# Kernel optimization log

Measured on AMD Instinct MI355X. Metric: run time of the kernel, lower is better.

The kernel has to match this reference:

```python
import jax, jax.numpy as jnp
import numpy as np

NF, NH1, NH21, NH22, NCLS = 6, 128, 128, 128, 3
OBS_X, OBS_Y, OBS_Z, R = 10.0, 10.0, 9.0, 7.0
BATCH = 131072


def setup_inputs() -> dict:
    key = jax.random.key(0)
    ks = jax.random.split(key, 16)
    def lin(kw, kb, fan_in, fan_out):
        bound = 1.0 / np.sqrt(fan_in)
        w = jax.random.uniform(kw, (fan_out, fan_in), jnp.float32, -bound, bound)
        b = jax.random.uniform(kb, (fan_out,), jnp.float32, -bound, bound)
        return w, b
    fc1_w, fc1_b = lin(ks[0], ks[1], NF, NH1)
    fc21_w, fc21_b = lin(ks[2], ks[3], NH1, NH21)
    fc22_w, fc22_b = lin(ks[4], ks[5], NH1, NH22)
    fcm1_w, fcm1_b = lin(ks[6], ks[7], NH21, NH21)
    fcm2_w, fcm2_b = lin(ks[8], ks[9], NH22, NH22)
    fc31_w, fc31_b = lin(ks[10], ks[11], NH21, NCLS)
    fc32_w, fc32_b = lin(ks[12], ks[13], NH22, 2)
    x = jax.random.normal(ks[14], (BATCH, NF), jnp.float32)
    mean = jnp.array([10.0, 0.0, 10.0, 0.0, 9.0, 0.0], jnp.float32)
    std = jnp.array([5.0, 2.0, 5.0, 2.0, 5.0, 2.0], jnp.float32)
    return {"x": x, "mean": mean, "std": std,
            "fc1_w": fc1_w, "fc1_b": fc1_b,
            "fc21_w": fc21_w, "fc21_b": fc21_b,
            "fc22_w": fc22_w, "fc22_b": fc22_b,
            "fcm1_w": fcm1_w, "fcm1_b": fcm1_b,
            "fcm2_w": fcm2_w, "fcm2_b": fcm2_b,
            "fc31_w": fc31_w, "fc31_b": fc31_b,
            "fc32_w": fc32_w, "fc32_b": fc32_b,
            "sgn": 1}


def _forward(x, mean, std, fc1_w, fc1_b, fc21_w, fc21_b, fc22_w, fc22_b,
             fcm1_w, fcm1_b, fcm2_w, fcm2_b, fc31_w, fc31_b, fc32_w, fc32_b):
    x0 = x * std + mean                                   # de-normalized state [B,6]
    h = jnp.tanh(x @ fc1_w.T + fc1_b)                     # [B,NH1]
    x21 = jnp.tanh(h @ fc21_w.T + fc21_b)
    x22 = jnp.tanh(h @ fc22_w.T + fc22_b)
    x21 = jnp.tanh(x21 @ fcm1_w.T + fcm1_b)
    x22 = jnp.tanh(x22 @ fcm2_w.T + fcm2_b)
    x31 = x21 @ fc31_w.T + fc31_b                         # QP linear term p, [B,3]
    x32 = 4.0 * jax.nn.sigmoid(x22 @ fc32_w.T + fc32_b)   # HOCBF penalties, [B,2]

    # higher-order CBF terms
    px, vx, py, vy, pz, vz = (x0[:, i] for i in range(6))
    dx, dy, dz = px - OBS_X, py - OBS_Y, pz - OBS_Z
    barrier = dx**4 + dy**4 + dz**4 - R**4
    barrier_dot = 4.0 * (dx**3 * vx + dy**3 * vy + dz**3 * vz)
    Lf2b = 12.0 * (dx**2 * vx**2 + dy**2 * vy**2 + dz**2 * vz**2)
    G = -4.0 * jnp.stack([dx**3, dy**3, dz**3], axis=-1)  # [B,3], single constraint G u <= h
    hvec = Lf2b + (x32[:, 0] + x32[:, 1]) * barrier_dot + x32[:, 0] * x32[:, 1] * barrier  # [B]

    # QP: min 0.5 u^T u + x31^T u  s.t.  G u <= h  (Q = I, one constraint)
    # Closed-form KKT: u = -x31 - lam*G, lam = max(0, (G @ (-x31) - h) / (G @ G))
    u_unc = -x31
    Gu = jnp.sum(G * u_unc, axis=-1)                      # [B]
    GG = jnp.sum(G * G, axis=-1)                          # [B]
    lam = jnp.maximum(Gu - hvec, 0.0) / GG
    u = u_unc - lam[:, None] * G                          # [B,3]
    return u


def reference(x, mean, std, fc1_w, fc1_b, fc21_w, fc21_b, fc22_w, fc22_b,
              fcm1_w, fcm1_b, fcm2_w, fcm2_b, fc31_w, fc31_b, fc32_w, fc32_b, sgn):
    return _forward(x, mean, std, fc1_w, fc1_b, fc21_w, fc21_b, fc22_w, fc22_b,
                    fcm1_w, fcm1_b, fcm2_w, fcm2_b, fc31_w, fc31_b, fc32_w, fc32_b)
```

## Files before the change

kernel.cpp:

```cpp
#include <hip/hip_runtime.h>

typedef _Float16 half8 __attribute__((ext_vector_type(8)));
typedef _Float16 half4_t __attribute__((ext_vector_type(4)));
typedef __fp16 fp16x2 __attribute__((ext_vector_type(2)));
typedef float float4_t __attribute__((ext_vector_type(4)));
typedef float float2_t __attribute__((ext_vector_type(2)));

#define SB 64
#define NT 512
#define RS (SB * 8)

#define OFF_W1   0
#define OFF_W21  4096
#define OFF_W22  20480
#define OFF_WM1  36864
#define OFF_WM2  53248
#define OFF_W4A  69632
#define OFF_BIAS 73728
#define WS_HELEMS 73728

#define SCL_TANH 2.8853900817779268f
#define SCL_SIG  -1.4426950408889634f

__device__ __forceinline__ float tanh_pre(float a) {
  float e = __builtin_amdgcn_exp2f(a);
  return fmaf(-2.f, __builtin_amdgcn_rcpf(1.f + e), 1.f);
}
__device__ __forceinline__ half4_t pack4(float v0, float v1, float v2, float v3) {
  fp16x2 lo = __builtin_amdgcn_cvt_pkrtz(v0, v1);
  fp16x2 hi = __builtin_amdgcn_cvt_pkrtz(v2, v3);
  half4_t h;
  h[0] = (_Float16)lo[0]; h[1] = (_Float16)lo[1];
  h[2] = (_Float16)hi[0]; h[3] = (_Float16)hi[1];
  return h;
}

__global__ void prepack(const float* __restrict__ w1, const float* __restrict__ w21,
                        const float* __restrict__ w22, const float* __restrict__ wm1,
                        const float* __restrict__ wm2, const float* __restrict__ w31,
                        const float* __restrict__ w32, const float* __restrict__ b1,
                        const float* __restrict__ b21, const float* __restrict__ b22,
                        const float* __restrict__ bm1, const float* __restrict__ bm2,
                        _Float16* __restrict__ ws) {
  const int stride = gridDim.x * blockDim.x;
  for (int i = blockIdx.x * blockDim.x + threadIdx.x; i < WS_HELEMS; i += stride) {
    float v;
    if (i < OFF_W21) {
      int t = i;
      int j = t & 7, c = t >> 3, l16 = c & 15, t1 = c >> 4;
      int k8 = t1 & 3, mt = t1 >> 2;
      int row = mt * 16 + l16, k = k8 * 8 + j;
      v = (k < 6) ? w1[row * 6 + k] * SCL_TANH : 0.f;
    } else if (i < OFF_W4A) {
      int t = i - OFF_W21;
      int m = t >> 14; t &= 16383;
      const float* src = (m == 0) ? w21 : (m == 1) ? w22 : (m == 2) ? wm1 : wm2;
      int j = t & 7, c = t >> 3, l16 = c & 15, t1 = c >> 4;
      int k8 = t1 & 15, mt = t1 >> 4;
      v = src[(mt * 16 + l16) * 128 + k8 * 8 + j] * SCL_TANH;
    } else {
      int t = i - OFF_W4A;
      int j = t & 7, r = t >> 3, l16 = r & 15, q = r >> 4;
      int cc = q & 15, chain = q >> 4;
      int k = cc * 8 + j, m = l16;
      if (chain == 0) v = (m < 3) ? w31[m * 128 + k] : 0.f;
      else            v = (m < 2) ? w32[m * 128 + k] * SCL_SIG : 0.f;
    }
    ws[i] = (_Float16)v;
  }
  float* bws = (float*)(ws + OFF_BIAS);
  for (int i = blockIdx.x * blockDim.x + threadIdx.x; i < 640; i += stride) {
    int layer = i >> 7, idx = i & 127;
    const float* src = (layer == 0) ? b1 : (layer == 1) ? b21
                     : (layer == 2) ? b22 : (layer == 3) ? bm1 : bm2;
    bws[i] = src[idx] * SCL_TANH;
  }
}

__device__ __forceinline__ void layer128(const half8* __restrict__ A, float4_t bv,
                                         const _Float16* __restrict__ inB,
                                         _Float16* __restrict__ outB,
                                         int quad, int l16, int wv) {
  float4_t acc[4];
  acc[0] = bv; acc[1] = bv; acc[2] = bv; acc[3] = bv;
#pragma unroll
  for (int kk = 0; kk < 4; ++kk) {
#pragma unroll
    for (int nt = 0; nt < 4; ++nt) {
      half8 b = *(const half8*)(inB + (kk * 4 + quad) * RS + (nt * 16 + l16) * 8);
      acc[nt] = __builtin_amdgcn_mfma_f32_16x16x32_f16(A[kk], b, acc[nt], 0, 0, 0);
    }
  }
  const int ob = wv * 16 + quad * 4;
  _Float16* base = outB + (ob >> 3) * RS + (ob & 7);
#pragma unroll
  for (int nt = 0; nt < 4; ++nt) {
    const int s = nt * 16 + l16;
    half4_t h = pack4(tanh_pre(acc[nt][0]), tanh_pre(acc[nt][1]),
                      tanh_pre(acc[nt][2]), tanh_pre(acc[nt][3]));
    *(half4_t*)(base + s * 8) = h;
  }
}

__global__ __launch_bounds__(NT, 3) void bnet_main(
    const float* __restrict__ x, const float* __restrict__ meang,
    const float* __restrict__ stdg, const float* __restrict__ b31,
    const float* __restrict__ b32, const _Float16* __restrict__ ws,
    float* __restrict__ out) {
  __shared__ __align__(16) _Float16 bufH[SB * 128];
  __shared__ __align__(16) _Float16 bufA[SB * 128];
  __shared__ __align__(16) _Float16 bufB[SB * 128];

  const int tid = threadIdx.x;
  const int wv = tid >> 6;
  const int lane = tid & 63;
  const int quad = lane >> 4;
  const int l16 = lane & 15;
  const int s0 = blockIdx.x * SB;
  const float* biasF = (const float*)(ws + OFF_BIAS);
  const int arow = (wv * 16 + quad * 4);

  half8 A1 = *(const half8*)(ws + OFF_W1 + ((wv * 4 + quad) * 16 + l16) * 8);
  float4_t bv1 = *(const float4_t*)(biasF + arow);
  float4_t bv21 = *(const float4_t*)(biasF + 128 + arow);
  float4_t bv22 = *(const float4_t*)(biasF + 256 + arow);
  float4_t bvm1 = *(const float4_t*)(biasF + 384 + arow);
  float4_t bvm2 = *(const float4_t*)(biasF + 512 + arow);
  half8 A21[4];
#pragma unroll
  for (int kk = 0; kk < 4; ++kk)
    A21[kk] = *(const half8*)(ws + OFF_W21 + ((wv * 16 + kk * 4 + quad) * 16 + l16) * 8);

  {
    float4_t acc[4];
    acc[0] = bv1; acc[1] = bv1; acc[2] = bv1; acc[3] = bv1;
#pragma unroll
    for (int nt = 0; nt < 4; ++nt) {
      half8 v;
#pragma unroll
      for (int j = 0; j < 8; ++j) v[j] = (_Float16)0.f;
      if (quad == 0) {
        const float* xp = x + (size_t)(s0 + nt * 16 + l16) * 6;
        float2_t e0 = *(const float2_t*)(xp);
        float2_t e1 = *(const float2_t*)(xp + 2);
        float2_t e2 = *(const float2_t*)(xp + 4);
        v[0] = (_Float16)e0[0]; v[1] = (_Float16)e0[1];
        v[2] = (_Float16)e1[0]; v[3] = (_Float16)e1[1];
        v[4] = (_Float16)e2[0]; v[5] = (_Float16)e2[1];
      }
      acc[nt] = __builtin_amdgcn_mfma_f32_16x16x32_f16(A1, v, acc[nt], 0, 0, 0);
    }
    _Float16* base = bufH + (arow >> 3) * RS + (arow & 7);
#pragma unroll
    for (int nt = 0; nt < 4; ++nt) {
      const int s = nt * 16 + l16;
      half4_t h = pack4(tanh_pre(acc[nt][0]), tanh_pre(acc[nt][1]),
                        tanh_pre(acc[nt][2]), tanh_pre(acc[nt][3]));
      *(half4_t*)(base + s * 8) = h;
    }
  }
  half8 A22[4];
#pragma unroll
  for (int kk = 0; kk < 4; ++kk)
    A22[kk] = *(const half8*)(ws + OFF_W22 + ((wv * 16 + kk * 4 + quad) * 16 + l16) * 8);
  __syncthreads();

  layer128(A21, bv21, bufH, bufA, quad, l16, wv);
  half8 AM1[4];
#pragma unroll
  for (int kk = 0; kk < 4; ++kk)
    AM1[kk] = *(const half8*)(ws + OFF_WM1 + ((wv * 16 + kk * 4 + quad) * 16 + l16) * 8);
  layer128(A22, bv22, bufH, bufB, quad, l16, wv);
  half8 AM2[4];
#pragma unroll
  for (int kk = 0; kk < 4; ++kk)
    AM2[kk] = *(const half8*)(ws + OFF_WM2 + ((wv * 16 + kk * 4 + quad) * 16 + l16) * 8);
  __syncthreads();

  layer128(AM1, bvm1, bufA, bufH, quad, l16, wv);
  half8 A4[2][4];
  if (wv < 4) {
#pragma unroll
    for (int c = 0; c < 2; ++c)
#pragma unroll
      for (int kk = 0; kk < 4; ++kk)
        A4[c][kk] = *(const half8*)(ws + OFF_W4A +
                                    ((c * 16 + kk * 4 + quad) * 16 + l16) * 8);
  }
  __syncthreads();

  layer128(AM2, bvm2, bufB, bufA, quad, l16, wv);
  __syncthreads();

  if (wv < 4) {
    const int nt = wv;
    float4_t c0 = (float4_t){0.f, 0.f, 0.f, 0.f};
    float4_t c1 = (float4_t){0.f, 0.f, 0.f, 0.f};
    if (quad == 0) {
      c0[0] = b31[0]; c0[1] = b31[1]; c0[2] = b31[2];
      c1[0] = b32[0] * SCL_SIG; c1[1] = b32[1] * SCL_SIG;
    }
#pragma unroll
    for (int kk = 0; kk < 4; ++kk) {
      half8 bh = *(const half8*)(bufH + (kk * 4 + quad) * RS + (nt * 16 + l16) * 8);
      half8 bc = *(const half8*)(bufA + (kk * 4 + quad) * RS + (nt * 16 + l16) * 8);
      c0 = __builtin_amdgcn_mfma_f32_16x16x32_f16(A4[0][kk], bh, c0, 0, 0, 0);
      c1 = __builtin_amdgcn_mfma_f32_16x16x32_f16(A4[1][kk], bc, c1, 0, 0, 0);
    }
    if (quad == 0) {
      const int s = nt * 16 + l16;
      float u0 = -c0[0];
      float u1 = -c0[1];
      float u2 = -c0[2];
      float p0 = 4.f * __builtin_amdgcn_rcpf(1.f + __builtin_amdgcn_exp2f(c1[0]));
      float p1 = 4.f * __builtin_amdgcn_rcpf(1.f + __builtin_amdgcn_exp2f(c1[1]));
      const float m0 = meang[0], m1 = meang[1], m2 = meang[2];
      const float m3 = meang[3], m4 = meang[4], m5 = meang[5];
      const float sd0 = stdg[0], sd1 = stdg[1], sd2 = stdg[2];
      const float sd3 = stdg[3], sd4 = stdg[4], sd5 = stdg[5];
      const float* xp = x + (size_t)(s0 + s) * 6;
      float2_t e0 = *(const float2_t*)(xp);
      float2_t e1 = *(const float2_t*)(xp + 2);
      float2_t e2 = *(const float2_t*)(xp + 4);
      float px = e0[0] * sd0 + m0, vx = e0[1] * sd1 + m1;
      float py = e1[0] * sd2 + m2, vy = e1[1] * sd3 + m3;
      float pz = e2[0] * sd4 + m4, vz = e2[1] * sd5 + m5;
      float dx = px - 10.f, dy = py - 10.f, dz = pz - 9.f;
      float dx2 = dx * dx, dy2 = dy * dy, dz2 = dz * dz;
      float dx3 = dx2 * dx, dy3 = dy2 * dy, dz3 = dz2 * dz;
      float barrier = dx3 * dx + dy3 * dy + dz3 * dz - 2401.f;
      float bdot = 4.f * (dx3 * vx + dy3 * vy + dz3 * vz);
      float Lf2b = 12.f * (dx2 * vx * vx + dy2 * vy * vy + dz2 * vz * vz);
      float g0 = -4.f * dx3, g1 = -4.f * dy3, g2 = -4.f * dz3;
      float hv = Lf2b + (p0 + p1) * bdot + p0 * p1 * barrier;
      float Gu = g0 * u0 + g1 * u1 + g2 * u2;
      float GG = g0 * g0 + g1 * g1 + g2 * g2;
      float lam = fmaxf(Gu - hv, 0.f) / GG;
      float* op = out + (size_t)(s0 + s) * 3;
      op[0] = u0 - lam * g0;
      op[1] = u1 - lam * g1;
      op[2] = u2 - lam * g2;
    }
  }
}

extern "C" void kernel_launch(void* const* d_in, const int* in_sizes, int n_in,
                              void* d_out, int out_size, void* d_ws, size_t ws_size,
                              hipStream_t stream) {
  const float* x    = (const float*)d_in[0];
  const float* mean = (const float*)d_in[1];
  const float* stdv = (const float*)d_in[2];
  const float* w1   = (const float*)d_in[3];
  const float* b1   = (const float*)d_in[4];
  const float* w21  = (const float*)d_in[5];
  const float* b21  = (const float*)d_in[6];
  const float* w22  = (const float*)d_in[7];
  const float* b22  = (const float*)d_in[8];
  const float* wm1  = (const float*)d_in[9];
  const float* bm1  = (const float*)d_in[10];
  const float* wm2  = (const float*)d_in[11];
  const float* bm2  = (const float*)d_in[12];
  const float* w31  = (const float*)d_in[13];
  const float* b31  = (const float*)d_in[14];
  const float* w32  = (const float*)d_in[15];
  const float* b32  = (const float*)d_in[16];
  _Float16* ws = (_Float16*)d_ws;
  float* out = (float*)d_out;
  const int batch = in_sizes[0] / 6;

  hipLaunchKernelGGL(prepack, dim3(96), dim3(256), 0, stream,
                     w1, w21, w22, wm1, wm2, w31, w32,
                     b1, b21, b22, bm1, bm2, ws);
  hipLaunchKernelGGL(bnet_main, dim3(batch / SB), dim3(NT), 0, stream,
                     x, mean, stdv, b31, b32, (const _Float16*)ws, out);
}
```

Before: 123.5 us.

## Restructure MLP so each wave owns 32 samples with LDS-staged weights

Changes the work split so that each wave computes all 128 output features for its own 32 samples, instead of every wave computing a 16-row output slice for the block's shared 64 samples. Layer weights are staged into double-buffered LDS, and the next layer's weights are loaded while the current layer runs. Activations stay in a private per-wave padded slab and are read back as MFMA fragments, which removes most of the inter-wave dependence on block-wide activation buffers. Each block now covers 256 samples, launch bounds drop to one block per CU, and the LDS footprint grows, so latency hiding rests on fewer resident waves.

```diff
diff --git a/kernel.cpp b/kernel.cpp
--- a/kernel.cpp
+++ b/kernel.cpp
@@ -6,9 +6,10 @@
 typedef float float4_t __attribute__((ext_vector_type(4)));
 typedef float float2_t __attribute__((ext_vector_type(2)));
 
-#define SB 64
 #define NT 512
-#define RS (SB * 8)
+#define SW 32
+#define SBLK 256
+#define P 136
 
 #define OFF_W1   0
 #define OFF_W21  4096
@@ -77,169 +78,191 @@
   }
 }
 
-__device__ __forceinline__ void layer128(const half8* __restrict__ A, float4_t bv,
-                                         const _Float16* __restrict__ inB,
-                                         _Float16* __restrict__ outB,
-                                         int quad, int l16, int wv) {
-  float4_t acc[4];
-  acc[0] = bv; acc[1] = bv; acc[2] = bv; acc[3] = bv;
-#pragma unroll
-  for (int kk = 0; kk < 4; ++kk) {
-#pragma unroll
-    for (int nt = 0; nt < 4; ++nt) {
-      half8 b = *(const half8*)(inB + (kk * 4 + quad) * RS + (nt * 16 + l16) * 8);
-      acc[nt] = __builtin_amdgcn_mfma_f32_16x16x32_f16(A[kk], b, acc[nt], 0, 0, 0);
-    }
-  }
-  const int ob = wv * 16 + quad * 4;
-  _Float16* base = outB + (ob >> 3) * RS + (ob & 7);
-#pragma unroll
-  for (int nt = 0; nt < 4; ++nt) {
-    const int s = nt * 16 + l16;
-    half4_t h = pack4(tanh_pre(acc[nt][0]), tanh_pre(acc[nt][1]),
-                      tanh_pre(acc[nt][2]), tanh_pre(acc[nt][3]));
-    *(half4_t*)(base + s * 8) = h;
-  }
-}
-
-__global__ __launch_bounds__(NT, 3) void bnet_main(
+__device__ __forceinline__ void stage32(const _Float16* __restrict__ src,
+                                        _Float16* __restrict__ dst, int tid) {
+#pragma unroll
+  for (int i = 0; i < 4; ++i)
+    *(half8*)(dst + (i * NT + tid) * 8) = *(const half8*)(src + (i * NT + tid) * 8);
+}
+__device__ __forceinline__ void stage8(const _Float16* __restrict__ src,
+                                       _Float16* __restrict__ dst, int tid) {
+  *(half8*)(dst + tid * 8) = *(const half8*)(src + tid * 8);
+}
+
+__device__ __forceinline__ void layer_big(const _Float16* __restrict__ wb,
+                                          const float* __restrict__ bbase,
+                                          const half8 (&bIn)[2][4],
+                                          _Float16* __restrict__ myslab,
+                                          int quad, int l16) {
+#pragma unroll
+  for (int m = 0; m < 8; ++m) {
+    float4_t bv = *(const float4_t*)(bbase + m * 16 + quad * 4);
+    float4_t a0 = bv, a1 = bv;
+#pragma unroll
+    for (int kk = 0; kk < 4; ++kk) {
+      half8 A = *(const half8*)(wb + ((m * 16 + kk * 4 + quad) * 16 + l16) * 8);
+      a0 = __builtin_amdgcn_mfma_f32_16x16x32_f16(A, bIn[0][kk], a0, 0, 0, 0);
+      a1 = __builtin_amdgcn_mfma_f32_16x16x32_f16(A, bIn[1][kk], a1, 0, 0, 0);
+    }
+    const int fo = m * 16 + quad * 4;
+    *(half4_t*)(myslab + l16 * P + fo) =
+        pack4(tanh_pre(a0[0]), tanh_pre(a0[1]), tanh_pre(a0[2]), tanh_pre(a0[3]));
+    *(half4_t*)(myslab + (16 + l16) * P + fo) =
+        pack4(tanh_pre(a1[0]), tanh_pre(a1[1]), tanh_pre(a1[2]), tanh_pre(a1[3]));
+  }
+}
+
+__device__ __forceinline__ void read_frags(const _Float16* __restrict__ myslab,
+                                           half8 (&bOut)[2][4], int quad, int l16) {
+  asm volatile("s_waitcnt lgkmcnt(0)" ::: "memory");
+  __builtin_amdgcn_sched_barrier(0);
+#pragma unroll
+  for (int n = 0; n < 2; ++n)
+#pragma unroll
+    for (int kk = 0; kk < 4; ++kk)
+      bOut[n][kk] = *(const half8*)(myslab + (n * 16 + l16) * P + kk * 32 + quad * 8);
+}
+
+__global__ __launch_bounds__(NT, 1) void bnet_main(
     const float* __restrict__ x, const float* __restrict__ meang,
     const float* __restrict__ stdg, const float* __restrict__ b31,
     const float* __restrict__ b32, const _Float16* __restrict__ ws,
     float* __restrict__ out) {
-  __shared__ __align__(16) _Float16 bufH[SB * 128];
-  __shared__ __align__(16) _Float16 bufA[SB * 128];
-  __shared__ __align__(16) _Float16 bufB[SB * 128];
+  __shared__ __align__(16) _Float16 wb0[16384];
+  __shared__ __align__(16) _Float16 wb1[16384];
+  __shared__ __align__(16) _Float16 slab[8 * SW * P];
+  __shared__ __align__(16) float bbuf[640];
 
   const int tid = threadIdx.x;
   const int wv = tid >> 6;
   const int lane = tid & 63;
   const int quad = lane >> 4;
   const int l16 = lane & 15;
-  const int s0 = blockIdx.x * SB;
+  const int s0w = blockIdx.x * SBLK + wv * SW;
   const float* biasF = (const float*)(ws + OFF_BIAS);
-  const int arow = (wv * 16 + quad * 4);
-
-  half8 A1 = *(const half8*)(ws + OFF_W1 + ((wv * 4 + quad) * 16 + l16) * 8);
-  float4_t bv1 = *(const float4_t*)(biasF + arow);
-  float4_t bv21 = *(const float4_t*)(biasF + 128 + arow);
-  float4_t bv22 = *(const float4_t*)(biasF + 256 + arow);
-  float4_t bvm1 = *(const float4_t*)(biasF + 384 + arow);
-  float4_t bvm2 = *(const float4_t*)(biasF + 512 + arow);
-  half8 A21[4];
-#pragma unroll
-  for (int kk = 0; kk < 4; ++kk)
-    A21[kk] = *(const half8*)(ws + OFF_W21 + ((wv * 16 + kk * 4 + quad) * 16 + l16) * 8);
+  _Float16* myslab = slab + wv * (SW * P);
+
+  stage8(ws + OFF_W1, wb0, tid);
+  stage32(ws + OFF_W21, wb1, tid);
+  bbuf[tid] = biasF[tid];
+  if (tid < 128) bbuf[512 + tid] = biasF[512 + tid];
+  __syncthreads();
+
+  half8 xb[2];
+#pragma unroll
+  for (int n = 0; n < 2; ++n) {
+#pragma unroll
+    for (int j = 0; j < 8; ++j) xb[n][j] = (_Float16)0.f;
+    if (quad == 0) {
+      const float* xp = x + (size_t)(s0w + n * 16 + l16) * 6;
+      float2_t e0 = *(const float2_t*)(xp);
+      float2_t e1 = *(const float2_t*)(xp + 2);
+      float2_t e2 = *(const float2_t*)(xp + 4);
+      xb[n][0] = (_Float16)e0[0]; xb[n][1] = (_Float16)e0[1];
+      xb[n][2] = (_Float16)e1[0]; xb[n][3] = (_Float16)e1[1];
+      xb[n][4] = (_Float16)e2[0]; xb[n][5] = (_Float16)e2[1];
+    }
+  }
+#pragma unroll
+  for (int m = 0; m < 8; ++m) {
+    float4_t bv = *(const float4_t*)(bbuf + m * 16 + quad * 4);
+    float4_t a0 = bv, a1 = bv;
+    half8 A = *(const half8*)(wb0 + ((m * 4 + quad) * 16 + l16) * 8);
+    a0 = __builtin_amdgcn_mfma_f32_16x16x32_f16(A, xb[0], a0, 0, 0, 0);
+    a1 = __builtin_amdgcn_mfma_f32_16x16x32_f16(A, xb[1], a1, 0, 0, 0);
+    const int fo = m * 16 + quad * 4;
+    *(half4_t*)(myslab + l16 * P + fo) =
+        pack4(tanh_pre(a0[0]), tanh_pre(a0[1]), tanh_pre(a0[2]), tanh_pre(a0[3]));
+    *(half4_t*)(myslab + (16 + l16) * P + fo) =
+        pack4(tanh_pre(a1[0]), tanh_pre(a1[1]), tanh_pre(a1[2]), tanh_pre(a1[3]));
+  }
+  half8 f_h[2][4];
+  read_frags(myslab, f_h, quad, l16);
+  __syncthreads();
+
+  stage32(ws + OFF_W22, wb0, tid);
+  layer_big(wb1, bbuf + 128, f_h, myslab, quad, l16);
+  half8 f_a[2][4];
+  read_frags(myslab, f_a, quad, l16);
+  __syncthreads();
+
+  stage32(ws + OFF_WM1, wb1, tid);
+  layer_big(wb0, bbuf + 256, f_h, myslab, quad, l16);
+  half8 f_b[2][4];
+  read_frags(myslab, f_b, quad, l16);
+  __syncthreads();
+
+  stage32(ws + OFF_WM2, wb0, tid);
+  layer_big(wb1, bbuf + 384, f_a, myslab, quad, l16);
+  read_frags(myslab, f_a, quad, l16);
+  __syncthreads();
+
+  stage8(ws + OFF_W4A, wb1, tid);
+  layer_big(wb0, bbuf + 512, f_b, myslab, quad, l16);
+  read_frags(myslab, f_b, quad, l16);
+  __syncthreads();
 
   {
-    float4_t acc[4];
-    acc[0] = bv1; acc[1] = bv1; acc[2] = bv1; acc[3] = bv1;
-#pragma unroll
-    for (int nt = 0; nt < 4; ++nt) {
-      half8 v;
-#pragma unroll
-      for (int j = 0; j < 8; ++j) v[j] = (_Float16)0.f;
+    half8 A40[4], A41[4];
+#pragma unroll
+    for (int kk = 0; kk < 4; ++kk) {
+      A40[kk] = *(const half8*)(wb1 + ((kk * 4 + quad) * 16 + l16) * 8);
+      A41[kk] = *(const half8*)(wb1 + ((16 + kk * 4 + quad) * 16 + l16) * 8);
+    }
+    float4_t c0[2], c1[2];
+#pragma unroll
+    for (int n = 0; n < 2; ++n) {
+      c0[n] = (float4_t){0.f, 0.f, 0.f, 0.f};
+      c1[n] = (float4_t){0.f, 0.f, 0.f, 0.f};
       if (quad == 0) {
-        const float* xp = x + (size_t)(s0 + nt * 16 + l16) * 6;
-        float2_t e0 = *(const float2_t*)(xp);
-        float2_t e1 = *(const float2_t*)(xp + 2);
-        float2_t e2 = *(const float2_t*)(xp + 4);
-        v[0] = (_Float16)e0[0]; v[1] = (_Float16)e0[1];
-        v[2] = (_Float16)e1[0]; v[3] = (_Float16)e1[1];
-        v[4] = (_Float16)e2[0]; v[5] = (_Float16)e2[1];
+        c0[n][0] = b31[0]; c0[n][1] = b31[1]; c0[n][2] = b31[2];
+        c1[n][0] = b32[0] * SCL_SIG; c1[n][1] = b32[1] * SCL_SIG;
       }
-      acc[nt] = __builtin_amdgcn_mfma_f32_16x16x32_f16(A1, v, acc[nt], 0, 0, 0);
-    }
-    _Float16* base = bufH + (arow >> 3) * RS + (arow & 7);
-#pragma unroll
-    for (int nt = 0; nt < 4; ++nt) {
-      const int s = nt * 16 + l16;
-      half4_t h = pack4(tanh_pre(acc[nt][0]), tanh_pre(acc[nt][1]),
-                        tanh_pre(acc[nt][2]), tanh_pre(acc[nt][3]));
-      *(half4_t*)(base + s * 8) = h;
-    }
-  }
-  half8 A22[4];
-#pragma unroll
-  for (int kk = 0; kk < 4; ++kk)
-    A22[kk] = *(const half8*)(ws + OFF_W22 + ((wv * 16 + kk * 4 + quad) * 16 + l16) * 8);
-  __syncthreads();
-
-  layer128(A21, bv21, bufH, bufA, quad, l16, wv);
-  half8 AM1[4];
-#pragma unroll
-  for (int kk = 0; kk < 4; ++kk)
-    AM1[kk] = *(const half8*)(ws + OFF_WM1 + ((wv * 16 + kk * 4 + quad) * 16 + l16) * 8);
-  layer128(A22, bv22, bufH, bufB, quad, l16, wv);
-  half8 AM2[4];
-#pragma unroll
-  for (int kk = 0; kk < 4; ++kk)
-    AM2[kk] = *(const half8*)(ws + OFF_WM2 + ((wv * 16 + kk * 4 + quad) * 16 + l16) * 8);
-  __syncthreads();
-
-  layer128(AM1, bvm1, bufA, bufH, quad, l16, wv);
-  half8 A4[2][4];
-  if (wv < 4) {
-#pragma unroll
-    for (int c = 0; c < 2; ++c)
-#pragma unroll
-      for (int kk = 0; kk < 4; ++kk)
-        A4[c][kk] = *(const half8*)(ws + OFF_W4A +
-                                    ((c * 16 + kk * 4 + quad) * 16 + l16) * 8);
-  }
-  __syncthreads();
-
-  layer128(AM2, bvm2, bufB, bufA, quad, l16, wv);
-  __syncthreads();
-
-  if (wv < 4) {
-    const int nt = wv;
-    float4_t c0 = (float4_t){0.f, 0.f, 0.f, 0.f};
-    float4_t c1 = (float4_t){0.f, 0.f, 0.f, 0.f};
+    }
+#pragma unroll
+    for (int kk = 0; kk < 4; ++kk) {
+#pragma unroll
+      for (int n = 0; n < 2; ++n) {
+        c0[n] = __builtin_amdgcn_mfma_f32_16x16x32_f16(A40[kk], f_a[n][kk], c0[n], 0, 0, 0);
+        c1[n] = __builtin_amdgcn_mfma_f32_16x16x32_f16(A41[kk], f_b[n][kk], c1[n], 0, 0, 0);
+      }
+    }
     if (quad == 0) {
-      c0[0] = b31[0]; c0[1] = b31[1]; c0[2] = b31[2];
-      c1[0] = b32[0] * SCL_SIG; c1[1] = b32[1] * SCL_SIG;
-    }
-#pragma unroll
-    for (int kk = 0; kk < 4; ++kk) {
-      half8 bh = *(const half8*)(bufH + (kk * 4 + quad) * RS + (nt * 16 + l16) * 8);
-      half8 bc = *(const half8*)(bufA + (kk * 4 + quad) * RS + (nt * 16 + l16) * 8);
-      c0 = __builtin_amdgcn_mfma_f32_16x16x32_f16(A4[0][kk], bh, c0, 0, 0, 0);
-      c1 = __builtin_amdgcn_mfma_f32_16x16x32_f16(A4[1][kk], bc, c1, 0, 0, 0);
-    }
-    if (quad == 0) {
-      const int s = nt * 16 + l16;
-      float u0 = -c0[0];
-      float u1 = -c0[1];
-      float u2 = -c0[2];
-      float p0 = 4.f * __builtin_amdgcn_rcpf(1.f + __builtin_amdgcn_exp2f(c1[0]));
-      float p1 = 4.f * __builtin_amdgcn_rcpf(1.f + __builtin_amdgcn_exp2f(c1[1]));
       const float m0 = meang[0], m1 = meang[1], m2 = meang[2];
       const float m3 = meang[3], m4 = meang[4], m5 = meang[5];
       const float sd0 = stdg[0], sd1 = stdg[1], sd2 = stdg[2];
       const float sd3 = stdg[3], sd4 = stdg[4], sd5 = stdg[5];
-      const float* xp = x + (size_t)(s0 + s) * 6;
-      float2_t e0 = *(const float2_t*)(xp);
-      float2_t e1 = *(const float2_t*)(xp + 2);
-      float2_t e2 = *(const float2_t*)(xp + 4);
-      float px = e0[0] * sd0 + m0, vx = e0[1] * sd1 + m1;
-      float py = e1[0] * sd2 + m2, vy = e1[1] * sd3 + m3;
-      float pz = e2[0] * sd4 + m4, vz = e2[1] * sd5 + m5;
-      float dx = px - 10.f, dy = py - 10.f, dz = pz - 9.f;
-      float dx2 = dx * dx, dy2 = dy * dy, dz2 = dz * dz;
-      float dx3 = dx2 * dx, dy3 = dy2 * dy, dz3 = dz2 * dz;
-      float barrier = dx3 * dx + dy3 * dy + dz3 * dz - 2401.f;
-      float bdot = 4.f * (dx3 * vx + dy3 * vy + dz3 * vz);
-      float Lf2b = 12.f * (dx2 * vx * vx + dy2 * vy * vy + dz2 * vz * vz);
-      float g0 = -4.f * dx3, g1 = -4.f * dy3, g2 = -4.f * dz3;
-      float hv = Lf2b + (p0 + p1) * bdot + p0 * p1 * barrier;
-      float Gu = g0 * u0 + g1 * u1 + g2 * u2;
-      float GG = g0 * g0 + g1 * g1 + g2 * g2;
-      float lam = fmaxf(Gu - hv, 0.f) / GG;
-      float* op = out + (size_t)(s0 + s) * 3;
-      op[0] = u0 - lam * g0;
-      op[1] = u1 - lam * g1;
-      op[2] = u2 - lam * g2;
+#pragma unroll
+      for (int n = 0; n < 2; ++n) {
+        const int s = s0w + n * 16 + l16;
+        float u0 = -c0[n][0];
+        float u1 = -c0[n][1];
+        float u2 = -c0[n][2];
+        float p0 = 4.f * __builtin_amdgcn_rcpf(1.f + __builtin_amdgcn_exp2f(c1[n][0]));
+        float p1 = 4.f * __builtin_amdgcn_rcpf(1.f + __builtin_amdgcn_exp2f(c1[n][1]));
+        const float* xp = x + (size_t)s * 6;
+        float2_t e0 = *(const float2_t*)(xp);
+        float2_t e1 = *(const float2_t*)(xp + 2);
+        float2_t e2 = *(const float2_t*)(xp + 4);
+        float px = e0[0] * sd0 + m0, vx = e0[1] * sd1 + m1;
+        float py = e1[0] * sd2 + m2, vy = e1[1] * sd3 + m3;
+        float pz = e2[0] * sd4 + m4, vz = e2[1] * sd5 + m5;
+        float dx = px - 10.f, dy = py - 10.f, dz = pz - 9.f;
+        float dx2 = dx * dx, dy2 = dy * dy, dz2 = dz * dz;
+        float dx3 = dx2 * dx, dy3 = dy2 * dy, dz3 = dz2 * dz;
+        float barrier = dx3 * dx + dy3 * dy + dz3 * dz - 2401.f;
+        float bdot = 4.f * (dx3 * vx + dy3 * vy + dz3 * vz);
+        float Lf2b = 12.f * (dx2 * vx * vx + dy2 * vy * vy + dz2 * vz * vz);
+        float g0 = -4.f * dx3, g1 = -4.f * dy3, g2 = -4.f * dz3;
+        float hv = Lf2b + (p0 + p1) * bdot + p0 * p1 * barrier;
+        float Gu = g0 * u0 + g1 * u1 + g2 * u2;
+        float GG = g0 * g0 + g1 * g1 + g2 * g2;
+        float lam = fmaxf(Gu - hv, 0.f) / GG;
+        float* op = out + (size_t)s * 3;
+        op[0] = u0 - lam * g0;
+        op[1] = u1 - lam * g1;
+        op[2] = u2 - lam * g2;
+      }
     }
   }
 }
@@ -271,6 +294,6 @@
   hipLaunchKernelGGL(prepack, dim3(96), dim3(256), 0, stream,
                      w1, w21, w22, wm1, wm2, w31, w32,
                      b1, b21, b22, bm1, bm2, ws);
-  hipLaunchKernelGGL(bnet_main, dim3(batch / SB), dim3(NT), 0, stream,
+  hipLaunchKernelGGL(bnet_main, dim3(batch / SBLK), dim3(NT), 0, stream,
                      x, mean, stdv, b31, b32, (const _Float16*)ws, out);
 }
```

After: 124.1 us. No clear change (+0.5%).

## Retile hidden layers as 2x2 MFMA warp tiles with just-in-time weight loads

Applied to the files above, without the earlier changes.

Each 128-wide hidden layer was split as one 16-row output tile per wave across all four 16-sample column tiles. It is now a 2x2 block per wave: two output-row tiles times two sample tiles. Each B fragment read from LDS now feeds two MFMAs, which halves LDS reads per MFMA. Weights and biases are loaded inside the layer instead of being prefetched one layer ahead, and the bias is added after accumulation. Occupancy hint drops from 3 to 2 blocks per CU, which gives more registers but exposes weight-load latency that prefetching used to hide.

```diff
diff --git a/kernel.cpp b/kernel.cpp
--- a/kernel.cpp
+++ b/kernel.cpp
@@ -77,32 +77,59 @@
   }
 }
 
-__device__ __forceinline__ void layer128(const half8* __restrict__ A, float4_t bv,
+__device__ __forceinline__ void layer2x2(const _Float16* __restrict__ wA,
+                                         const float* __restrict__ bb,
                                          const _Float16* __restrict__ inB,
                                          _Float16* __restrict__ outB,
-                                         int quad, int l16, int wv) {
-  float4_t acc[4];
-  acc[0] = bv; acc[1] = bv; acc[2] = bv; acc[3] = bv;
-#pragma unroll
-  for (int kk = 0; kk < 4; ++kk) {
-#pragma unroll
-    for (int nt = 0; nt < 4; ++nt) {
-      half8 b = *(const half8*)(inB + (kk * 4 + quad) * RS + (nt * 16 + l16) * 8);
-      acc[nt] = __builtin_amdgcn_mfma_f32_16x16x32_f16(A[kk], b, acc[nt], 0, 0, 0);
-    }
-  }
-  const int ob = wv * 16 + quad * 4;
-  _Float16* base = outB + (ob >> 3) * RS + (ob & 7);
-#pragma unroll
-  for (int nt = 0; nt < 4; ++nt) {
-    const int s = nt * 16 + l16;
-    half4_t h = pack4(tanh_pre(acc[nt][0]), tanh_pre(acc[nt][1]),
-                      tanh_pre(acc[nt][2]), tanh_pre(acc[nt][3]));
-    *(half4_t*)(base + s * 8) = h;
-  }
-}
-
-__global__ __launch_bounds__(NT, 3) void bnet_main(
+                                         int mg, int ng, int quad, int l16) {
+  const int mt0 = mg * 2;
+  half8 A[2][4];
+#pragma unroll
+  for (int mi = 0; mi < 2; ++mi)
+#pragma unroll
+    for (int kk = 0; kk < 4; ++kk)
+      A[mi][kk] = *(const half8*)(wA + (((mt0 + mi) * 16 + kk * 4 + quad) * 16 + l16) * 8);
+  float4_t bv[2];
+  bv[0] = *(const float4_t*)(bb + (mt0 + 0) * 16 + quad * 4);
+  bv[1] = *(const float4_t*)(bb + (mt0 + 1) * 16 + quad * 4);
+
+  float4_t acc[2][2];
+#pragma unroll
+  for (int mi = 0; mi < 2; ++mi)
+#pragma unroll
+    for (int ni = 0; ni < 2; ++ni)
+      acc[mi][ni] = (float4_t){0.f, 0.f, 0.f, 0.f};
+
+#pragma unroll
+  for (int ni = 0; ni < 2; ++ni) {
+    const int nt = ng * 2 + ni;
+    half8 B[4];
+#pragma unroll
+    for (int kk = 0; kk < 4; ++kk)
+      B[kk] = *(const half8*)(inB + (kk * 4 + quad) * RS + (nt * 16 + l16) * 8);
+#pragma unroll
+    for (int kk = 0; kk < 4; ++kk) {
+      acc[0][ni] = __builtin_amdgcn_mfma_f32_16x16x32_f16(A[0][kk], B[kk], acc[0][ni], 0, 0, 0);
+      acc[1][ni] = __builtin_amdgcn_mfma_f32_16x16x32_f16(A[1][kk], B[kk], acc[1][ni], 0, 0, 0);
+    }
+  }
+
+#pragma unroll
+  for (int mi = 0; mi < 2; ++mi) {
+    const int ob = (mt0 + mi) * 16 + quad * 4;
+    _Float16* base = outB + (ob >> 3) * RS + (ob & 7);
+#pragma unroll
+    for (int ni = 0; ni < 2; ++ni) {
+      const int s = (ng * 2 + ni) * 16 + l16;
+      float4_t a = acc[mi][ni];
+      half4_t h = pack4(tanh_pre(a[0] + bv[mi][0]), tanh_pre(a[1] + bv[mi][1]),
+                        tanh_pre(a[2] + bv[mi][2]), tanh_pre(a[3] + bv[mi][3]));
+      *(half4_t*)(base + s * 8) = h;
+    }
+  }
+}
+
+__global__ __launch_bounds__(NT, 2) void bnet_main(
     const float* __restrict__ x, const float* __restrict__ meang,
     const float* __restrict__ stdg, const float* __restrict__ b31,
     const float* __restrict__ b32, const _Float16* __restrict__ ws,
@@ -116,68 +143,64 @@
   const int lane = tid & 63;
   const int quad = lane >> 4;
   const int l16 = lane & 15;
+  const int mg = wv >> 1;
+  const int ng = wv & 1;
   const int s0 = blockIdx.x * SB;
   const float* biasF = (const float*)(ws + OFF_BIAS);
-  const int arow = (wv * 16 + quad * 4);
-
-  half8 A1 = *(const half8*)(ws + OFF_W1 + ((wv * 4 + quad) * 16 + l16) * 8);
-  float4_t bv1 = *(const float4_t*)(biasF + arow);
-  float4_t bv21 = *(const float4_t*)(biasF + 128 + arow);
-  float4_t bv22 = *(const float4_t*)(biasF + 256 + arow);
-  float4_t bvm1 = *(const float4_t*)(biasF + 384 + arow);
-  float4_t bvm2 = *(const float4_t*)(biasF + 512 + arow);
-  half8 A21[4];
-#pragma unroll
-  for (int kk = 0; kk < 4; ++kk)
-    A21[kk] = *(const half8*)(ws + OFF_W21 + ((wv * 16 + kk * 4 + quad) * 16 + l16) * 8);
 
   {
-    float4_t acc[4];
-    acc[0] = bv1; acc[1] = bv1; acc[2] = bv1; acc[3] = bv1;
-#pragma unroll
-    for (int nt = 0; nt < 4; ++nt) {
-      half8 v;
-#pragma unroll
-      for (int j = 0; j < 8; ++j) v[j] = (_Float16)0.f;
+    half8 A1[2];
+#pragma unroll
+    for (int mi = 0; mi < 2; ++mi)
+      A1[mi] = *(const half8*)(ws + OFF_W1 + (((mg * 2 + mi) * 4 + quad) * 16 + l16) * 8);
+    float4_t bv1[2];
+    bv1[0] = *(const float4_t*)(biasF + (mg * 2 + 0) * 16 + quad * 4);
+    bv1[1] = *(const float4_t*)(biasF + (mg * 2 + 1) * 16 + quad * 4);
+
+    half8 xb[2];
+#pragma unroll
+    for (int ni = 0; ni < 2; ++ni) {
+#pragma unroll
+      for (int j = 0; j < 8; ++j) xb[ni][j] = (_Float16)0.f;
       if (quad == 0) {
-        const float* xp = x + (size_t)(s0 + nt * 16 + l16) * 6;
+        const float* xp = x + (size_t)(s0 + (ng * 2 + ni) * 16 + l16) * 6;
         float2_t e0 = *(const float2_t*)(xp);
         float2_t e1 = *(const float2_t*)(xp + 2);
         float2_t e2 = *(const float2_t*)(xp + 4);
-        v[0] = (_Float16)e0[0]; v[1] = (_Float16)e0[1];
-        v[2] = (_Float16)e1[0]; v[3] = (_Float16)e1[1];
-        v[4] = (_Float16)e2[0]; v[5] = (_Float16)e2[1];
+        xb[ni][0] = (_Float16)e0[0]; xb[ni][1] = (_Float16)e0[1];
+        xb[ni][2] = (_Float16)e1[0]; xb[ni][3] = (_Float16)e1[1];
+        xb[ni][4] = (_Float16)e2[0]; xb[ni][5] = (_Float16)e2[1];
       }
-      acc[nt] = __builtin_amdgcn_mfma_f32_16x16x32_f16(A1, v, acc[nt], 0, 0, 0);
-    }
-    _Float16* base = bufH + (arow >> 3) * RS + (arow & 7);
-#pragma unroll
-    for (int nt = 0; nt < 4; ++nt) {
-      const int s = nt * 16 + l16;
-      half4_t h = pack4(tanh_pre(acc[nt][0]), tanh_pre(acc[nt][1]),
-                        tanh_pre(acc[nt][2]), tanh_pre(acc[nt][3]));
-      *(half4_t*)(base + s * 8) = h;
-    }
-  }
-  half8 A22[4];
-#pragma unroll
-  for (int kk = 0; kk < 4; ++kk)
-    A22[kk] = *(const half8*)(ws + OFF_W22 + ((wv * 16 + kk * 4 + quad) * 16 + l16) * 8);
-  __syncthreads();
-
-  layer128(A21, bv21, bufH, bufA, quad, l16, wv);
-  half8 AM1[4];
-#pragma unroll
-  for (int kk = 0; kk < 4; ++kk)
-    AM1[kk] = *(const half8*)(ws + OFF_WM1 + ((wv * 16 + kk * 4 + quad) * 16 + l16) * 8);
-  layer128(A22, bv22, bufH, bufB, quad, l16, wv);
-  half8 AM2[4];
-#pragma unroll
-  for (int kk = 0; kk < 4; ++kk)
-    AM2[kk] = *(const half8*)(ws + OFF_WM2 + ((wv * 16 + kk * 4 + quad) * 16 + l16) * 8);
-  __syncthreads();
-
-  layer128(AM1, bvm1, bufA, bufH, quad, l16, wv);
+    }
+    float4_t acc[2][2];
+#pragma unroll
+    for (int mi = 0; mi < 2; ++mi)
+#pragma unroll
+      for (int ni = 0; ni < 2; ++ni) {
+        acc[mi][ni] = (float4_t){0.f, 0.f, 0.f, 0.f};
+        acc[mi][ni] = __builtin_amdgcn_mfma_f32_16x16x32_f16(A1[mi], xb[ni], acc[mi][ni], 0, 0, 0);
+      }
+#pragma unroll
+    for (int mi = 0; mi < 2; ++mi) {
+      const int ob = (mg * 2 + mi) * 16 + quad * 4;
+      _Float16* base = bufH + (ob >> 3) * RS + (ob & 7);
+#pragma unroll
+      for (int ni = 0; ni < 2; ++ni) {
+        const int s = (ng * 2 + ni) * 16 + l16;
+        float4_t a = acc[mi][ni];
+        half4_t h = pack4(tanh_pre(a[0] + bv1[mi][0]), tanh_pre(a[1] + bv1[mi][1]),
+                          tanh_pre(a[2] + bv1[mi][2]), tanh_pre(a[3] + bv1[mi][3]));
+        *(half4_t*)(base + s * 8) = h;
+      }
+    }
+  }
+  __syncthreads();
+
+  layer2x2(ws + OFF_W21, biasF + 128, bufH, bufA, mg, ng, quad, l16);
+  layer2x2(ws + OFF_W22, biasF + 256, bufH, bufB, mg, ng, quad, l16);
+  __syncthreads();
+
+  layer2x2(ws + OFF_WM1, biasF + 384, bufA, bufH, mg, ng, quad, l16);
   half8 A4[2][4];
   if (wv < 4) {
 #pragma unroll
@@ -189,7 +212,7 @@
   }
   __syncthreads();
 
-  layer128(AM2, bvm2, bufB, bufA, quad, l16, wv);
+  layer2x2(ws + OFF_WM2, biasF + 512, bufB, bufA, mg, ng, quad, l16);
   __syncthreads();
 
   if (wv < 4) {
```

Measured after the change: 126.9 us. +2.7%, slower.
